# Kernel tuning notes

Hardware: AMD Instinct MI355X
Metric: run time of the kernel (lower is better)

## Reference

```python
import jax, jax.numpy as jnp
import numpy as np

HQ, HK, DH = 32, 8, 64
ROPE_BASE = 10000.0


def _rope_tables(T, dtype):
    pos = jnp.arange(T, dtype=jnp.float32)
    inv_freq = 1.0 / (ROPE_BASE ** (jnp.arange(0, DH, 2, dtype=jnp.float32) / DH))
    freqs = pos[:, None] * inv_freq[None, :]          # (T, DH/2)
    cos = jnp.concatenate([jnp.cos(freqs), jnp.cos(freqs)], -1).astype(dtype)  # (T, DH)
    sin = jnp.concatenate([jnp.sin(freqs), jnp.sin(freqs)], -1).astype(dtype)
    return cos, sin


def _rotate_half(t):
    return jnp.concatenate([-t[..., DH // 2:], t[..., :DH // 2]], -1)


def setup_inputs() -> dict:
    key = jax.random.key(0)
    k1, k2, k3, k4 = jax.random.split(key, 4)
    B, T, D = 2, 2048, 2048
    std = 0.02 / np.sqrt(24)
    kv_std = std / np.sqrt(HQ / HK)
    return {
        "x": jax.random.normal(k1, (B, T, D), jnp.float32),
        "Wq": jax.random.normal(k2, (D, HQ * DH), jnp.float32) * std,
        "Wkv": jax.random.normal(k3, (D, 2 * HK * DH), jnp.float32) * kv_std,
        "Wo": jax.random.normal(k4, (HQ * DH, D), jnp.float32) * std,
    }


def reference(x, Wq, Wkv, Wo):
    B, T, D = x.shape
    g = HQ // HK
    scale = DH ** -0.5
    # projections
    q = (x @ Wq).reshape(B, T, HQ, DH).transpose(0, 2, 1, 3)       # (B,Hq,T,Dh)
    kv = (x @ Wkv).reshape(B, T, 2, HK, DH)
    k = kv[:, :, 0].transpose(0, 2, 1, 3)                           # (B,Hk,T,Dh)
    v = kv[:, :, 1].transpose(0, 2, 1, 3)
    # GQA expand: each kv head repeated g times consecutively
    k = jnp.repeat(k, g, axis=1)                                    # (B,Hq,T,Dh)
    v = jnp.repeat(v, g, axis=1)
    # RoPE on q and repeated k
    cos, sin = _rope_tables(T, x.dtype)
    q = q * cos + _rotate_half(q) * sin
    k = k * cos + _rotate_half(k) * sin
    # attention
    scores = jnp.einsum('bhqd,bhkd->bhqk', q, k) * scale            # (B,Hq,T,T)
    causal = jnp.triu(jnp.ones((T, T), bool), 1)
    scores = jnp.where(causal, -jnp.inf, scores)
    attn = jax.nn.softmax(scores.astype(jnp.float32), axis=-1).astype(x.dtype)
    out = jnp.einsum('bhqk,bhkd->bhqd', attn, v)                    # (B,Hq,T,Dh)
    out = out.transpose(0, 2, 1, 3).reshape(B, T, HQ * DH)
    return out @ Wo
```

## Files before the change

kernel.cpp:

```cpp
#include <hip/hip_runtime.h>
#include <hip/hip_bf16.h>

#define DEVI __device__ __forceinline__

typedef __attribute__((ext_vector_type(4))) float f32x4;
typedef __attribute__((ext_vector_type(16))) float f32x16;
typedef __attribute__((ext_vector_type(8))) short s16x8;
typedef __attribute__((ext_vector_type(4))) short s16x4;
typedef __attribute__((ext_vector_type(2))) unsigned u32x2;

DEVI ushort f2bf(float f) {
  union { float f; unsigned u; } v; v.f = f;
  unsigned r = v.u + 0x7FFFu + ((v.u >> 16) & 1u);
  return (ushort)(r >> 16);
}

DEVI void gload_lds16(const void* g, void* l) {
  __builtin_amdgcn_global_load_lds((const __attribute__((address_space(1))) void*)g,
                                   (__attribute__((address_space(3))) void*)l, 16, 0, 0);
}

#define MFMA16 __builtin_amdgcn_mfma_f32_16x16x32_bf16
#define SBAR() __builtin_amdgcn_s_barrier()
#define LGKM0() asm volatile("s_waitcnt lgkmcnt(0)")

DEVI float plswap_max(float x) {
  union { float f; unsigned u; } a; a.f = x;
  u32x2 r = __builtin_amdgcn_permlane32_swap(a.u, a.u, false, false);
  union { unsigned u; float f; } o0, o1; o0.u = r[0]; o1.u = r[1];
  return fmaxf(o0.f, o1.f);
}
DEVI float plswap_sum(float x) {
  union { float f; unsigned u; } a; a.f = x;
  u32x2 r = __builtin_amdgcn_permlane32_swap(a.u, a.u, false, false);
  union { unsigned u; float f; } o0, o1; o0.u = r[0]; o1.u = r[1];
  return o0.f + o1.f;
}

DEVI void stage128q(const ushort* __restrict__ gsrc, int K, ushort* ld, int tid) {
  #pragma unroll
  for (int j = 0; j < 4; ++j) {
    const int ci = j * 256 + tid;
    const int row = ci >> 3, c = ci & 7;
    gload_lds16(gsrc + (size_t)row * K + ((c ^ (row & 7)) << 3),
                ld + (size_t)(j * 256 + (tid & ~63)) * 8);
  }
}
DEVI void stage256q(const ushort* __restrict__ gsrc, int K, ushort* ld, int tid) {
  #pragma unroll
  for (int j = 0; j < 8; ++j) {
    const int ci = j * 256 + tid;
    const int row = ci >> 3, c = ci & 7;
    gload_lds16(gsrc + (size_t)row * K + ((c ^ (row & 7)) << 3),
                ld + (size_t)(j * 256 + (tid & ~63)) * 8);
  }
}
DEVI s16x8 ldfrag(const ushort* tile, int row, int kc) {
  return *(const s16x8*)((const char*)tile + row * 128 + ((kc ^ (row & 7)) << 4));
}

DEVI void kloop3(const ushort* __restrict__ A, const ushort* __restrict__ BT,
                 ushort* Asm, ushort* Bsm, int m0, int n0, int K, int NKT,
                 f32x4 (&acc)[4][4], int tid, int wm, int wn, int g, int l15) {
  stage128q(A + (size_t)m0 * K, K, Asm, tid);
  stage128q(BT + (size_t)n0 * K, K, Bsm, tid);
  stage128q(BT + (size_t)n0 * K + 64, K, Bsm + 8192, tid);
  asm volatile("s_waitcnt vmcnt(4)");
  SBAR();

  int rd = 0;
  #pragma unroll 1
  for (int t = 0; t < NKT; ++t) {
    const ushort* Ah = Asm + (t & 1) * 8192;
    const ushort* Bh = Bsm + rd * 8192;
    s16x8 af[4][2], bfr[4][2];

    #pragma unroll
    for (int ks = 0; ks < 2; ++ks) {
      #pragma unroll
      for (int ni = 0; ni < 4; ++ni)
        bfr[ni][ks] = ldfrag(Bh, wn * 64 + ni * 16 + l15, ks * 4 + g);
      #pragma unroll
      for (int mi = 0; mi < 4; ++mi)
        af[mi][ks] = ldfrag(Ah, wm * 64 + mi * 16 + l15, ks * 4 + g);
    }
    if (t + 1 < NKT)
      stage128q(A + (size_t)m0 * K + (t + 1) * 64, K, Asm + ((t + 1) & 1) * 8192, tid);
    int wr = rd + 2; if (wr >= 3) wr -= 3;
    if (t + 2 < NKT)
      stage128q(BT + (size_t)n0 * K + (t + 2) * 64, K, Bsm + wr * 8192, tid);

    LGKM0();
    __builtin_amdgcn_sched_barrier(0);
    __builtin_amdgcn_s_setprio(1);
    #pragma unroll
    for (int mi = 0; mi < 4; ++mi)
      #pragma unroll
      for (int ni = 0; ni < 2; ++ni)
        #pragma unroll
        for (int ks = 0; ks < 2; ++ks)
          acc[mi][ni] = MFMA16(af[mi][ks], bfr[ni][ks], acc[mi][ni], 0, 0, 0);
    #pragma unroll
    for (int mi = 0; mi < 4; ++mi)
      #pragma unroll
      for (int ni = 0; ni < 2; ++ni)
        #pragma unroll
        for (int ks = 0; ks < 2; ++ks)
          acc[mi][2 + ni] = MFMA16(af[mi][ks], bfr[2 + ni][ks], acc[mi][2 + ni], 0, 0, 0);
    __builtin_amdgcn_s_setprio(0);

    if (t + 2 < NKT)      asm volatile("s_waitcnt vmcnt(4)");
    else if (t + 1 < NKT) asm volatile("s_waitcnt vmcnt(0)");
    SBAR();
    rd = (rd == 2) ? 0 : rd + 1;
  }
}

__global__ __launch_bounds__(256) void cast_bf16_k(const float* __restrict__ in,
                                                   ushort* __restrict__ out, int n) {
  int i = (blockIdx.x * 256 + threadIdx.x) * 4;
  if (i >= n) return;
  float4 v = *(const float4*)(in + i);
  ushort4 o;
  o.x = f2bf(v.x); o.y = f2bf(v.y); o.z = f2bf(v.z); o.w = f2bf(v.w);
  *(ushort4*)(out + i) = o;
}

__global__ __launch_bounds__(256) void transpose_cast_k(const float* __restrict__ in,
                                                        ushort* __restrict__ out, int R, int C) {
  __shared__ ushort tile[64][66];
  const int r0 = blockIdx.y * 64, c0 = blockIdx.x * 64;
  const int tid = threadIdx.x;
  #pragma unroll
  for (int j = 0; j < 16; ++j) {
    int idx = j * 256 + tid;
    int r = idx >> 6, c = idx & 63;
    tile[c][r] = f2bf(in[(size_t)(r0 + r) * C + c0 + c]);
  }
  __syncthreads();
  #pragma unroll
  for (int j = 0; j < 16; ++j) {
    int idx = j * 256 + tid;
    int c = idx >> 6, r = idx & 63;
    out[(size_t)(c0 + c) * R + r0 + r] = tile[c][r];
  }
}

__global__ __launch_bounds__(256) void rope_table_k(float2* __restrict__ tab) {
  int idx = blockIdx.x * 256 + threadIdx.x;
  int t = idx >> 5, i = idx & 31;
  float inv = expf(-(float)i * 0.28782313662425575f);
  float ang = (float)t * inv;
  tab[idx] = make_float2(cosf(ang), sinf(ang));
}

__global__ __attribute__((amdgpu_flat_work_group_size(256, 256)))
__attribute__((amdgpu_waves_per_eu(1, 1)))
void gemm_qkv_fat(const ushort* __restrict__ A,
                  const ushort* __restrict__ BT,
                  const float2* __restrict__ tab,
                  ushort* __restrict__ Qp,
                  ushort* __restrict__ Kp,
                  ushort* __restrict__ Vp) {
  constexpr int K = 2048, NKT = 32, GX = 24, NWG = 384;
  __shared__ __attribute__((aligned(128))) ushort smem[57344];
  ushort* Asm = smem;
  ushort* Bsm = smem + 32768;
  ushort* Ot = smem;

  const int tid = threadIdx.x;
  const int ln = tid & 63, wv = tid >> 6;
  const int g = ln >> 4, l15 = ln & 15, l31 = ln & 31, hi = ln >> 5;
  const int wm = wv >> 1, wn = wv & 1;

  const int orig = blockIdx.x;
  const int wg = (orig & 7) * (NWG / 8) + (orig >> 3);
  const int bx = wg % GX, by = wg / GX;
  const int m0 = by * 256, n0 = bx * 128;

  f32x4 acc[8][4];
  #pragma unroll
  for (int i = 0; i < 8; ++i)
    #pragma unroll
    for (int j = 0; j < 4; ++j) acc[i][j] = (f32x4){0.f, 0.f, 0.f, 0.f};

  stage256q(A + (size_t)m0 * K, K, Asm, tid);
  stage128q(BT + (size_t)n0 * K, K, Bsm, tid);
  stage128q(BT + (size_t)n0 * K + 64, K, Bsm + 8192, tid);
  asm volatile("s_waitcnt vmcnt(4)");
  SBAR();

  int rd = 0;
  #pragma unroll 1
  for (int t = 0; t < NKT; ++t) {
    const ushort* Ah = Asm + (t & 1) * 16384;
    const ushort* Bh = Bsm + rd * 8192;

    if (t + 1 < NKT)
      stage256q(A + (size_t)m0 * K + (t + 1) * 64, K, Asm + ((t + 1) & 1) * 16384, tid);
    int wr = rd + 2; if (wr >= 3) wr -= 3;
    if (t + 2 < NKT)
      stage128q(BT + (size_t)n0 * K + (t + 2) * 64, K, Bsm + wr * 8192, tid);

    #pragma unroll
    for (int ks = 0; ks < 2; ++ks) {
      s16x8 af[8], bfr[4];
      #pragma unroll
      for (int ni = 0; ni < 4; ++ni)
        bfr[ni] = ldfrag(Bh, wn * 64 + ni * 16 + l15, ks * 4 + g);
      #pragma unroll
      for (int mi = 0; mi < 8; ++mi)
        af[mi] = ldfrag(Ah, wm * 128 + mi * 16 + l15, ks * 4 + g);
      LGKM0();
      __builtin_amdgcn_sched_barrier(0);
      __builtin_amdgcn_s_setprio(1);
      #pragma unroll
      for (int mi = 0; mi < 8; ++mi)
        #pragma unroll
        for (int ni = 0; ni < 4; ++ni)
          acc[mi][ni] = MFMA16(af[mi], bfr[ni], acc[mi][ni], 0, 0, 0);
      __builtin_amdgcn_s_setprio(0);
    }

    if (t + 2 < NKT)      asm volatile("s_waitcnt vmcnt(4)");
    else if (t + 1 < NKT) asm volatile("s_waitcnt vmcnt(0)");
    SBAR();
    rd = (rd == 2) ? 0 : rd + 1;
  }

  __syncthreads();
  const int bq = by >> 3;
  const int tb0 = (by & 7) * 256;
  const int type = (bx < 16) ? 0 : (bx < 20 ? 1 : 2);
  constexpr int OST = 132;

  #pragma unroll
  for (int mi = 0; mi < 8; ++mi)
    #pragma unroll
    for (int r = 0; r < 4; ++r) {
      const int tl = wm * 128 + mi * 16 + g * 4 + r;
      const int t = tb0 + tl;
      #pragma unroll
      for (int ni = 0; ni < 4; ++ni) {
        const int cl = wn * 64 + ni * 16 + l15;
        float val = acc[mi][ni][r];
        float outv;
        if (type < 2) {
          float pairv = acc[mi][ni ^ 2][r];
          float2 cs = tab[t * 32 + (ni & 1) * 16 + l15];
          outv = (ni & 2) ? (val * cs.x + pairv * cs.y) : (val * cs.x - pairv * cs.y);
          if (type == 0) outv *= 0.18033688011112042f;
        } else {
          outv = val;
        }
        Ot[tl * OST + cl] = f2bf(outv);
      }
    }
  __syncthreads();

  #pragma unroll
  for (int it = 0; it < 16; ++it) {
    const int id = wv * 16 + it;
    const int hl = id >> 5, q8 = (id >> 2) & 7, fi = id & 3;
    const int tile = (by & 7) * 8 + q8;
    if (type < 2) {
      const ushort* srow = Ot + (q8 * 32 + l31) * OST + hl * 64 + fi * 16 + hi * 8;
      union { s16x4 h[2]; s16x8 v; } u;
      u.h[0] = *(const s16x4*)srow;
      u.h[1] = *(const s16x4*)(srow + 4);
      ushort* dst;
      if (type == 0) {
        const int h = bx * 2 + hl;
        dst = Qp + (((size_t)(bq * 32 + h) * 64 + tile) * 4 + fi) * 512 + ln * 8;
      } else {
        const int h = (bx - 16) * 2 + hl;
        dst = Kp + (((size_t)(bq * 8 + h) * 64 + tile) * 4 + fi) * 512 + ln * 8;
      }
      *(s16x8*)dst = u.v;
    } else {
      const int hk = (bx - 20) * 2 + hl;
      const int col = hl * 64 + (fi & 1) * 32 + l31;
      const int row0 = q8 * 32 + (fi >> 1) * 16 + hi * 8;
      ushort o[8];
      #pragma unroll
      for (int j2 = 0; j2 < 8; ++j2) o[j2] = Ot[(row0 + j2) * OST + col];
      ushort* dst = Vp + (((size_t)(bq * 8 + hk) * 64 + tile) * 4 + fi) * 512 + ln * 8;
      *(s16x8*)dst = *(const s16x8*)o;
    }
  }
}

__global__ __launch_bounds__(256) void gemm_bt_3b(const ushort* __restrict__ A,
                                                  const ushort* __restrict__ BT,
                                                  float* __restrict__ C, int M, int N, int K) {
  __shared__ __attribute__((aligned(128))) ushort smem[40960];
  ushort* Asm = smem;
  ushort* Bsm = smem + 16384;

  const int tid = threadIdx.x;
  const int ln = tid & 63, wv = tid >> 6;
  const int g = ln >> 4, l15 = ln & 15;
  const int wm = wv >> 1, wn = wv & 1;
  const int m0 = blockIdx.y * 128, n0 = blockIdx.x * 128;
  const int NKT = K / 64;

  f32x4 acc[4][4];
  #pragma unroll
  for (int i = 0; i < 4; ++i)
    #pragma unroll
    for (int j = 0; j < 4; ++j) acc[i][j] = (f32x4){0.f, 0.f, 0.f, 0.f};

  kloop3(A, BT, Asm, Bsm, m0, n0, K, NKT, acc, tid, wm, wn, g, l15);

  #pragma unroll
  for (int mi = 0; mi < 4; ++mi)
    #pragma unroll
    for (int r = 0; r < 4; ++r) {
      int row = m0 + wm * 64 + mi * 16 + g * 4 + r;
      float* crow = C + (size_t)row * N + n0 + wn * 64 + l15;
      #pragma unroll
      for (int ni = 0; ni < 4; ++ni) crow[ni * 16] = acc[mi][ni][r];
    }
}

__global__ __launch_bounds__(256) void attn_k(const ushort* __restrict__ Qp,
                                              const ushort* __restrict__ Kp,
                                              const ushort* __restrict__ Vp,
                                              ushort* __restrict__ O) {
  __shared__ ushort ep[4][32 * 64];
  const int tid = threadIdx.x, wv = tid >> 6, ln = tid & 63;
  const int l31 = ln & 31, hi = ln >> 5;

  const int f = blockIdx.x + gridDim.x * (blockIdx.y + 32 * blockIdx.z);
  const int xcd = f & 7, j = f >> 3;
  const int pr = xcd + 8 * (j & 1);
  const int b = pr >> 3, hk = pr & 7;
  const int s = j >> 1;
  const int hq = hk * 4 + (s & 3);
  const int qtile = 63 - ((s >> 2) * 4 + wv);
  const int qw = qtile * 32;
  const int nt = qtile + 1;

  const ushort* Qh    = Qp + ((size_t)(b * 32 + hq)) * (64 * 2048);
  const ushort* Kbase = Kp + ((size_t)(b * 8 + hk)) * (64 * 2048);
  const ushort* Vbase = Vp + ((size_t)(b * 8 + hk)) * (64 * 2048);
  ushort* lds = ep[wv];

  s16x8 qf[4];
  {
    const ushort* qp_ = Qh + (size_t)qtile * 2048 + ln * 8;
    #pragma unroll
    for (int ks = 0; ks < 4; ++ks) qf[ks] = *(const s16x8*)(qp_ + ks * 512);
  }

  f32x16 z16;
  #pragma unroll
  for (int r = 0; r < 16; ++r) z16[r] = 0.f;

  f32x16 oacc[2];
  #pragma unroll
  for (int dt = 0; dt < 2; ++dt)
    #pragma unroll
    for (int r = 0; r < 16; ++r) oacc[dt][r] = 0.f;
  float m = -1e30f, l = 0.f;

  const ushort* kp = Kbase + ln * 8;
  const ushort* vp = Vbase + ln * 8;

  s16x8 kf[4];
  #pragma unroll
  for (int ks = 0; ks < 4; ++ks) kf[ks] = *(const s16x8*)(kp + ks * 512);
  kp += 2048;

  s16x8 vc[4];
  union pfu { unsigned u[4]; s16x8 v; };
  pfu pf0, pf1;

  #pragma unroll 1
  for (int kt = 0; kt < nt; ++kt) {
    if (kt) {
      __builtin_amdgcn_s_setprio(1);
      oacc[0] = __builtin_amdgcn_mfma_f32_32x32x16_bf16(vc[0], pf0.v, oacc[0], 0, 0, 0);
      oacc[1] = __builtin_amdgcn_mfma_f32_32x32x16_bf16(vc[1], pf0.v, oacc[1], 0, 0, 0);
      oacc[0] = __builtin_amdgcn_mfma_f32_32x32x16_bf16(vc[2], pf1.v, oacc[0], 0, 0, 0);
      oacc[1] = __builtin_amdgcn_mfma_f32_32x32x16_bf16(vc[3], pf1.v, oacc[1], 0, 0, 0);
      __builtin_amdgcn_s_setprio(0);
    }
    #pragma unroll
    for (int fi2 = 0; fi2 < 4; ++fi2) vc[fi2] = *(const s16x8*)(vp + fi2 * 512);
    vp += 2048;

    __builtin_amdgcn_s_setprio(1);
    f32x16 sp = __builtin_amdgcn_mfma_f32_32x32x16_bf16(kf[0], qf[0], z16, 0, 0, 0);
    sp = __builtin_amdgcn_mfma_f32_32x32x16_bf16(kf[1], qf[1], sp, 0, 0, 0);
    sp = __builtin_amdgcn_mfma_f32_32x32x16_bf16(kf[2], qf[2], sp, 0, 0, 0);
    sp = __builtin_amdgcn_mfma_f32_32x32x16_bf16(kf[3], qf[3], sp, 0, 0, 0);
    __builtin_amdgcn_s_setprio(0);

    if (kt + 1 < nt) {
      #pragma unroll
      for (int ks = 0; ks < 4; ++ks) kf[ks] = *(const s16x8*)(kp + ks * 512);
      kp += 2048;
    }

    if (kt == qtile) {
      #pragma unroll
      for (int r = 0; r < 16; ++r) {
        int key = (r & 3) + 8 * (r >> 2) + 4 * hi;
        if (key > l31) sp[r] = -1e30f;
      }
    }

    float t0 = fmaxf(fmaxf(sp[0], sp[1]), sp[2]);
    float t1 = fmaxf(fmaxf(sp[3], sp[4]), sp[5]);
    float t2 = fmaxf(fmaxf(sp[6], sp[7]), sp[8]);
    float t3 = fmaxf(fmaxf(sp[9], sp[10]), sp[11]);
    float t4 = fmaxf(fmaxf(sp[12], sp[13]), sp[14]);
    float u0 = fmaxf(fmaxf(t0, t1), t2);
    float u1 = fmaxf(fmaxf(t3, t4), sp[15]);
    float pm = plswap_max(fmaxf(u0, u1));

    if (__any(pm - m > 8.0f)) {
      float mn = fmaxf(m, pm);
      float alpha = __builtin_amdgcn_exp2f(m - mn);
      m = mn;
      l *= alpha;
      #pragma unroll
      for (int dt = 0; dt < 2; ++dt)
        #pragma unroll
        for (int r = 0; r < 16; ++r) oacc[dt][r] *= alpha;
    }

    #pragma unroll
    for (int r = 0; r < 16; ++r) sp[r] = __builtin_amdgcn_exp2f(sp[r] - m);
    {
      float a0 = sp[0] + sp[1], a1 = sp[2] + sp[3], a2 = sp[4] + sp[5], a3 = sp[6] + sp[7];
      float a4 = sp[8] + sp[9], a5 = sp[10] + sp[11], a6 = sp[12] + sp[13], a7 = sp[14] + sp[15];
      float b0 = a0 + a1, b1 = a2 + a3, b2 = a4 + a5, b3 = a6 + a7;
      l += plswap_sum((b0 + b1) + (b2 + b3));
    }

    unsigned cw[8];
    #pragma unroll
    for (int jj = 0; jj < 8; ++jj) {
      union { __hip_bfloat162 h; unsigned u; } pk;
      pk.h = __float22bfloat162_rn(make_float2(sp[2 * jj], sp[2 * jj + 1]));
      cw[jj] = pk.u;
    }
    {
      u32x2 r;
      r = __builtin_amdgcn_permlane32_swap(cw[0], cw[2], false, false);
      pf0.u[0] = r[0]; pf0.u[2] = r[1];
      r = __builtin_amdgcn_permlane32_swap(cw[1], cw[3], false, false);
      pf0.u[1] = r[0]; pf0.u[3] = r[1];
      r = __builtin_amdgcn_permlane32_swap(cw[4], cw[6], false, false);
      pf1.u[0] = r[0]; pf1.u[2] = r[1];
      r = __builtin_amdgcn_permlane32_swap(cw[5], cw[7], false, false);
      pf1.u[1] = r[0]; pf1.u[3] = r[1];
    }
  }

  __builtin_amdgcn_s_setprio(1);
  oacc[0] = __builtin_amdgcn_mfma_f32_32x32x16_bf16(vc[0], pf0.v, oacc[0], 0, 0, 0);
  oacc[1] = __builtin_amdgcn_mfma_f32_32x32x16_bf16(vc[1], pf0.v, oacc[1], 0, 0, 0);
  oacc[0] = __builtin_amdgcn_mfma_f32_32x32x16_bf16(vc[2], pf1.v, oacc[0], 0, 0, 0);
  oacc[1] = __builtin_amdgcn_mfma_f32_32x32x16_bf16(vc[3], pf1.v, oacc[1], 0, 0, 0);
  __builtin_amdgcn_s_setprio(0);

  float invl = 1.0f / l;
  #pragma unroll
  for (int dt = 0; dt < 2; ++dt)
    #pragma unroll
    for (int r = 0; r < 16; ++r) {
      int d = dt * 32 + (r & 3) + 8 * (r >> 2) + 4 * hi;
      int byte = (l31 * 128 + d * 2) ^ ((l31 & 7) << 4);
      *(ushort*)((char*)lds + byte) = f2bf(oacc[dt][r] * invl);
    }
  const int qr = ln >> 1, half = ln & 1;
  #pragma unroll
  for (int jj = 0; jj < 4; ++jj) {
    int byte = (qr * 128 + half * 64 + jj * 16) ^ ((qr & 7) << 4);
    s16x8 vrow = *(const s16x8*)((const char*)lds + byte);
    *(s16x8*)(O + ((size_t)(b * 2048 + qw + qr)) * 2048 + hq * 64 + half * 32 + jj * 8) = vrow;
  }
}

extern "C" void kernel_launch(void* const* d_in, const int* in_sizes, int n_in,
                              void* d_out, int out_size, void* d_ws, size_t ws_size,
                              hipStream_t stream) {
  const float* x   = (const float*)d_in[0];
  const float* Wq  = (const float*)d_in[1];
  const float* Wkv = (const float*)d_in[2];
  const float* Wo  = (const float*)d_in[3];
  float* out = (float*)d_out;

  char* ws = (char*)d_ws;
  ushort* xb     = (ushort*)(ws);
  ushort* WqkvT  = (ushort*)(ws + 16777216);
  ushort* WoT    = (ushort*)(ws + 29360128);
  float2* tab    = (float2*)(ws + 37748736);
  ushort* Qp     = (ushort*)(ws + 38273024);
  ushort* Kp     = (ushort*)(ws + 55050240);
  ushort* Vp     = (ushort*)(ws + 59244544);
  ushort* Ob     = (ushort*)(ws + 63438848);

  cast_bf16_k<<<8192, 256, 0, stream>>>(x, xb, 2 * 2048 * 2048);
  transpose_cast_k<<<dim3(32, 32), 256, 0, stream>>>(Wq, WqkvT, 2048, 2048);
  transpose_cast_k<<<dim3(16, 32), 256, 0, stream>>>(Wkv, WqkvT + 2048 * 2048, 2048, 1024);
  transpose_cast_k<<<dim3(32, 32), 256, 0, stream>>>(Wo, WoT, 2048, 2048);
  rope_table_k<<<256, 256, 0, stream>>>(tab);
  gemm_qkv_fat<<<384, 256, 0, stream>>>(xb, WqkvT, tab, Qp, Kp, Vp);
  attn_k<<<dim3(16, 32, 2), 256, 0, stream>>>(Qp, Kp, Vp, Ob);
  gemm_bt_3b<<<dim3(16, 32), 256, 0, stream>>>(Ob, WoT, out, 4096, 2048, 2048);
}
```

Measured before the change: 236.5 us.

## Enlarge QKV GEMM tile to 256x256 with 512-thread workgroups

The fused QKV projection GEMM moves from 256x128 tiles with 4 waves to 256x256 tiles with 8 waves, halving the grid to 192 workgroups. B staging now uses 512 threads, and the LDS is enlarged to hold a triple-buffered 256-wide B tile. The RoPE/scale epilogue is split into two passes over 128-row halves so the output staging fits in LDS. The aim is more operand reuse per loaded byte. The trade-off is that 192 workgroups may underfill the 256 CUs and leave the tail unbalanced.

```diff
diff --git a/kernel.cpp b/kernel.cpp
--- a/kernel.cpp
+++ b/kernel.cpp
@@ -46,13 +46,13 @@
                 ld + (size_t)(j * 256 + (tid & ~63)) * 8);
   }
 }
-DEVI void stage256q(const ushort* __restrict__ gsrc, int K, ushort* ld, int tid) {
-  #pragma unroll
-  for (int j = 0; j < 8; ++j) {
-    const int ci = j * 256 + tid;
+DEVI void stage256w(const ushort* __restrict__ gsrc, int K, ushort* ld, int tid) {
+  #pragma unroll
+  for (int j = 0; j < 4; ++j) {
+    const int ci = j * 512 + tid;
     const int row = ci >> 3, c = ci & 7;
     gload_lds16(gsrc + (size_t)row * K + ((c ^ (row & 7)) << 3),
-                ld + (size_t)(j * 256 + (tid & ~63)) * 8);
+                ld + (size_t)(j * 512 + (tid & ~63)) * 8);
   }
 }
 DEVI s16x8 ldfrag(const ushort* tile, int row, int kc) {
@@ -154,29 +154,28 @@
   tab[idx] = make_float2(cosf(ang), sinf(ang));
 }
 
-__global__ __attribute__((amdgpu_flat_work_group_size(256, 256)))
-__attribute__((amdgpu_waves_per_eu(1, 1)))
-void gemm_qkv_fat(const ushort* __restrict__ A,
-                  const ushort* __restrict__ BT,
-                  const float2* __restrict__ tab,
-                  ushort* __restrict__ Qp,
-                  ushort* __restrict__ Kp,
-                  ushort* __restrict__ Vp) {
-  constexpr int K = 2048, NKT = 32, GX = 24, NWG = 384;
-  __shared__ __attribute__((aligned(128))) ushort smem[57344];
+__global__ __attribute__((amdgpu_flat_work_group_size(512, 512)))
+__attribute__((amdgpu_waves_per_eu(2, 2)))
+void gemm_qkv_f256(const ushort* __restrict__ A,
+                   const ushort* __restrict__ BT,
+                   const float2* __restrict__ tab,
+                   ushort* __restrict__ Qp,
+                   ushort* __restrict__ Kp,
+                   ushort* __restrict__ Vp) {
+  constexpr int K = 2048, NKT = 32, GX = 12, NWG = 192;
+  __shared__ __attribute__((aligned(128))) ushort smem[81920];
   ushort* Asm = smem;
   ushort* Bsm = smem + 32768;
-  ushort* Ot = smem;
 
   const int tid = threadIdx.x;
   const int ln = tid & 63, wv = tid >> 6;
   const int g = ln >> 4, l15 = ln & 15, l31 = ln & 31, hi = ln >> 5;
-  const int wm = wv >> 1, wn = wv & 1;
+  const int wm = wv >> 2, wn = wv & 3;
 
   const int orig = blockIdx.x;
   const int wg = (orig & 7) * (NWG / 8) + (orig >> 3);
   const int bx = wg % GX, by = wg / GX;
-  const int m0 = by * 256, n0 = bx * 128;
+  const int m0 = by * 256, n0 = bx * 256;
 
   f32x4 acc[8][4];
   #pragma unroll
@@ -184,9 +183,9 @@
     #pragma unroll
     for (int j = 0; j < 4; ++j) acc[i][j] = (f32x4){0.f, 0.f, 0.f, 0.f};
 
-  stage256q(A + (size_t)m0 * K, K, Asm, tid);
-  stage128q(BT + (size_t)n0 * K, K, Bsm, tid);
-  stage128q(BT + (size_t)n0 * K + 64, K, Bsm + 8192, tid);
+  stage256w(A + (size_t)m0 * K, K, Asm, tid);
+  stage256w(BT + (size_t)n0 * K, K, Bsm, tid);
+  stage256w(BT + (size_t)n0 * K + 64, K, Bsm + 16384, tid);
   asm volatile("s_waitcnt vmcnt(4)");
   SBAR();
 
@@ -194,13 +193,13 @@
   #pragma unroll 1
   for (int t = 0; t < NKT; ++t) {
     const ushort* Ah = Asm + (t & 1) * 16384;
-    const ushort* Bh = Bsm + rd * 8192;
+    const ushort* Bh = Bsm + rd * 16384;
 
     if (t + 1 < NKT)
-      stage256q(A + (size_t)m0 * K + (t + 1) * 64, K, Asm + ((t + 1) & 1) * 16384, tid);
+      stage256w(A + (size_t)m0 * K + (t + 1) * 64, K, Asm + ((t + 1) & 1) * 16384, tid);
     int wr = rd + 2; if (wr >= 3) wr -= 3;
     if (t + 2 < NKT)
-      stage128q(BT + (size_t)n0 * K + (t + 2) * 64, K, Bsm + wr * 8192, tid);
+      stage256w(BT + (size_t)n0 * K + (t + 2) * 64, K, Bsm + wr * 16384, tid);
 
     #pragma unroll
     for (int ks = 0; ks < 2; ++ks) {
@@ -228,65 +227,69 @@
     rd = (rd == 2) ? 0 : rd + 1;
   }
 
-  __syncthreads();
   const int bq = by >> 3;
   const int tb0 = (by & 7) * 256;
-  const int type = (bx < 16) ? 0 : (bx < 20 ? 1 : 2);
-  constexpr int OST = 132;
-
-  #pragma unroll
-  for (int mi = 0; mi < 8; ++mi)
-    #pragma unroll
-    for (int r = 0; r < 4; ++r) {
-      const int tl = wm * 128 + mi * 16 + g * 4 + r;
-      const int t = tb0 + tl;
-      #pragma unroll
-      for (int ni = 0; ni < 4; ++ni) {
-        const int cl = wn * 64 + ni * 16 + l15;
-        float val = acc[mi][ni][r];
-        float outv;
-        if (type < 2) {
-          float pairv = acc[mi][ni ^ 2][r];
-          float2 cs = tab[t * 32 + (ni & 1) * 16 + l15];
-          outv = (ni & 2) ? (val * cs.x + pairv * cs.y) : (val * cs.x - pairv * cs.y);
-          if (type == 0) outv *= 0.18033688011112042f;
+  const int type = (bx < 8) ? 0 : (bx < 10 ? 1 : 2);
+  constexpr int OST = 260;
+
+  __syncthreads();
+  #pragma unroll 1
+  for (int hm = 0; hm < 2; ++hm) {
+    if (wm == hm) {
+      #pragma unroll
+      for (int mi = 0; mi < 8; ++mi)
+        #pragma unroll
+        for (int r = 0; r < 4; ++r) {
+          const int tl = mi * 16 + g * 4 + r;
+          const int t = tb0 + hm * 128 + tl;
+          #pragma unroll
+          for (int ni = 0; ni < 4; ++ni) {
+            const int cl = wn * 64 + ni * 16 + l15;
+            float val = acc[mi][ni][r], outv;
+            if (type < 2) {
+              float pairv = acc[mi][ni ^ 2][r];
+              float2 cs = tab[t * 32 + (ni & 1) * 16 + l15];
+              outv = (ni & 2) ? (val * cs.x + pairv * cs.y) : (val * cs.x - pairv * cs.y);
+              if (type == 0) outv *= 0.18033688011112042f;
+            } else {
+              outv = val;
+            }
+            smem[tl * OST + cl] = f2bf(outv);
+          }
+        }
+    }
+    __syncthreads();
+    #pragma unroll
+    for (int it = 0; it < 8; ++it) {
+      const int id = wv * 8 + it;
+      const int hl = id >> 4, q4 = (id >> 2) & 3, fi = id & 3;
+      const int tile = (by & 7) * 8 + hm * 4 + q4;
+      if (type < 2) {
+        const ushort* srow = smem + (q4 * 32 + l31) * OST + hl * 64 + fi * 16 + hi * 8;
+        union { s16x4 h[2]; s16x8 v; } u;
+        u.h[0] = *(const s16x4*)srow;
+        u.h[1] = *(const s16x4*)(srow + 4);
+        ushort* dst;
+        if (type == 0) {
+          const int h = bx * 4 + hl;
+          dst = Qp + (((size_t)(bq * 32 + h) * 64 + tile) * 4 + fi) * 512 + ln * 8;
         } else {
-          outv = val;
+          const int h = (bx - 8) * 4 + hl;
+          dst = Kp + (((size_t)(bq * 8 + h) * 64 + tile) * 4 + fi) * 512 + ln * 8;
         }
-        Ot[tl * OST + cl] = f2bf(outv);
+        *(s16x8*)dst = u.v;
+      } else {
+        const int hk = (bx - 10) * 4 + hl;
+        const int col = hl * 64 + (fi & 1) * 32 + l31;
+        const int row0 = q4 * 32 + (fi >> 1) * 16 + hi * 8;
+        union { ushort o[8]; s16x8 v; } u;
+        #pragma unroll
+        for (int j2 = 0; j2 < 8; ++j2) u.o[j2] = smem[(row0 + j2) * OST + col];
+        ushort* dst = Vp + (((size_t)(bq * 8 + hk) * 64 + tile) * 4 + fi) * 512 + ln * 8;
+        *(s16x8*)dst = u.v;
       }
     }
-  __syncthreads();
-
-  #pragma unroll
-  for (int it = 0; it < 16; ++it) {
-    const int id = wv * 16 + it;
-    const int hl = id >> 5, q8 = (id >> 2) & 7, fi = id & 3;
-    const int tile = (by & 7) * 8 + q8;
-    if (type < 2) {
-      const ushort* srow = Ot + (q8 * 32 + l31) * OST + hl * 64 + fi * 16 + hi * 8;
-      union { s16x4 h[2]; s16x8 v; } u;
-      u.h[0] = *(const s16x4*)srow;
-      u.h[1] = *(const s16x4*)(srow + 4);
-      ushort* dst;
-      if (type == 0) {
-        const int h = bx * 2 + hl;
-        dst = Qp + (((size_t)(bq * 32 + h) * 64 + tile) * 4 + fi) * 512 + ln * 8;
-      } else {
-        const int h = (bx - 16) * 2 + hl;
-        dst = Kp + (((size_t)(bq * 8 + h) * 64 + tile) * 4 + fi) * 512 + ln * 8;
-      }
-      *(s16x8*)dst = u.v;
-    } else {
-      const int hk = (bx - 20) * 2 + hl;
-      const int col = hl * 64 + (fi & 1) * 32 + l31;
-      const int row0 = q8 * 32 + (fi >> 1) * 16 + hi * 8;
-      ushort o[8];
-      #pragma unroll
-      for (int j2 = 0; j2 < 8; ++j2) o[j2] = Ot[(row0 + j2) * OST + col];
-      ushort* dst = Vp + (((size_t)(bq * 8 + hk) * 64 + tile) * 4 + fi) * 512 + ln * 8;
-      *(s16x8*)dst = *(const s16x8*)o;
-    }
+    __syncthreads();
   }
 }
 
@@ -509,7 +512,7 @@
   transpose_cast_k<<<dim3(16, 32), 256, 0, stream>>>(Wkv, WqkvT + 2048 * 2048, 2048, 1024);
   transpose_cast_k<<<dim3(32, 32), 256, 0, stream>>>(Wo, WoT, 2048, 2048);
   rope_table_k<<<256, 256, 0, stream>>>(tab);
-  gemm_qkv_fat<<<384, 256, 0, stream>>>(xb, WqkvT, tab, Qp, Kp, Vp);
+  gemm_qkv_f256<<<192, 512, 0, stream>>>(xb, WqkvT, tab, Qp, Kp, Vp);
   attn_k<<<dim3(16, 32, 2), 256, 0, stream>>>(Qp, Kp, Vp, Ob);
   gemm_bt_3b<<<dim3(16, 32), 256, 0, stream>>>(Ob, WoT, out, 4096, 2048, 2048);
 }
```

Measured after the change: 276.7 us. 1.17x slower.
